# Kernel optimization log

Measured on AMD Instinct MI355X. Metric: run time of the kernel, lower is better.

The kernel has to match this reference:

```python
import jax, jax.numpy as jnp
import numpy as np

B, CI, CO = 2, 32, 32
NX, NY, NZ = 64, 64, 64
M1, M2, M3 = 8, 8, 8
ZH = NZ // 2 + 1


def _dft_mat(N, sign):
    # Dense DFT twiddle matrix W[k, n] = exp(sign * 2j*pi*k*n/N), complex64.
    a = jnp.arange(N)
    ph = (sign * 2.0) * jnp.pi * jnp.outer(a, a).astype(jnp.float32) / N
    return jnp.exp(1j * ph)


def setup_inputs() -> dict:
    key = jax.random.key(0)
    ks = jax.random.split(key, 9)
    scale = 1.0 / (CI * CO)
    x = jax.random.normal(ks[0], (B, CI, NX, NY, NZ), dtype=jnp.float32)
    wshape = (CI, CO, M1, M2, M3)
    names = ['w1r', 'w1i', 'w2r', 'w2i', 'w3r', 'w3i', 'w4r', 'w4i']
    out = {'x': x}
    for i, nm in enumerate(names):
        out[nm] = scale * jax.random.uniform(ks[i + 1], wshape, dtype=jnp.float32)
    return out


def _dht3(x):
    # Naive O(N^2)-per-axis 3D DFT via dense matmuls; return real part.
    Wx = _dft_mat(NX, -1)
    Wy = _dft_mat(NY, -1)
    Wz = _dft_mat(NZ, -1)
    y = x.astype(jnp.complex64)
    y = jnp.einsum('bcxyz,xa->bcayz', y, Wx)
    y = jnp.einsum('bcxyz,ya->bcxaz', y, Wy)
    y = jnp.einsum('bcxyz,za->bcxya', y, Wz)
    return y.real


def _idht3(X):
    # Inverse DFT via dense matmuls; rectangular (ZH -> NZ) on last axis.
    Wxi = _dft_mat(NX, +1) / NX
    Wyi = _dft_mat(NY, +1) / NY
    kz = jnp.arange(ZH)
    nz = jnp.arange(NZ)
    Wzi = jnp.exp(1j * (2.0 * jnp.pi * jnp.outer(kz, nz).astype(jnp.float32) / NZ)) / NZ
    y = jnp.einsum('bcxyz,xa->bcayz', X, Wxi)
    y = jnp.einsum('bcxyz,ya->bcxaz', y, Wyi)
    y = jnp.einsum('bcxyz,za->bcxya', y, Wzi)
    return y.real


def _mul(a, b):
    # compl_mul3d: contract over input channels in the mode block.
    return jnp.einsum('bixyz,ioxyz->boxyz', a, b)


def reference(x, w1r, w1i, w2r, w2i, w3r, w3i, w4r, w4i):
    w1 = w1r + 1j * w1i
    w2 = w2r + 1j * w2i
    w3 = w3r + 1j * w3i
    w4 = w4r + 1j * w4i

    xd = _dht3(x)  # [B, CI, NX, NY, NZ] real

    out = jnp.zeros((B, CO, NX, NY, ZH), dtype=jnp.complex64)
    out = out.at[:, :, :M1, :M2, :M3].set(_mul(xd[:, :, :M1, :M2, :M3], w1))
    out = out.at[:, :, NX - M1:, :M2, :M3].set(_mul(xd[:, :, NX - M1:, :M2, :M3], w2))
    out = out.at[:, :, :M1, NY - M2:, :M3].set(_mul(xd[:, :, :M1, NY - M2:, :M3], w3))
    out = out.at[:, :, NX - M1:, NY - M2:, :M3].set(_mul(xd[:, :, NX - M1:, NY - M2:, :M3], w4))

    return _idht3(out)  # [B, CO, NX, NY, NZ] real
```

## Files before the change

### kernel.cpp

```cpp
#include <hip/hip_runtime.h>

#define PI2_64 0.098174770424681038f


__global__ __launch_bounds__(256) void k_fwd_zy(const float* __restrict__ x,
                                                float* __restrict__ z2) {
  __shared__ __align__(16) float sp[64 * 65];
  __shared__ __align__(8) float2 Zc[64 * 9];
  __shared__ __align__(8) float2 Ec[32 * 9], Oc[32 * 9];
  __shared__ __align__(8) float2 cs[64];
  int tid = threadIdx.x;

  const float4* xg = (const float4*)(x + (long)blockIdx.x * 4096);
#pragma unroll
  for (int j = 0; j < 4; ++j) {
    int idx = j * 256 + tid;
    float4 v = xg[idx];
    int flat = idx << 2;
    int y = flat >> 6, z = flat & 63;
    float* d = &sp[y * 65 + z];
    d[0] = v.x; d[1] = v.y; d[2] = v.z; d[3] = v.w;
  }
  if (tid < 64) {
    float s, c; __sincosf(PI2_64 * (float)tid, &s, &c);
    cs[tid] = make_float2(c, s);
  }
  __syncthreads();

  {
    int y = tid >> 2, qp = tid & 3;
    const float* row = &sp[y * 65];
    float Sr[8] = {0,0,0,0,0,0,0,0}, So[8] = {0,0,0,0,0,0,0,0};
    int p0 = qp * 8 + 1, pend = (qp == 3) ? 32 : (p0 + 8);
    for (int p = p0; p < pend; ++p) {
      float a = row[p], b = row[64 - p];
      float e = a + b, o = a - b;
      Sr[0] += e;
      int m = p & 63;
#pragma unroll
      for (int k = 1; k < 8; ++k) {
        float2 t = cs[m];
        Sr[k] = fmaf(e, t.x, Sr[k]);
        So[k] = fmaf(o, t.y, So[k]);
        m = (m + p) & 63;
      }
    }
    if (qp == 3) {
      float x0 = row[0], x32 = row[32];
      float a = x0 + x32, b = x0 - x32;
#pragma unroll
      for (int k = 0; k < 8; ++k) Sr[k] += (k & 1) ? b : a;
    }
#pragma unroll
    for (int k = 0; k < 8; ++k) {
      Sr[k] += __shfl_xor(Sr[k], 1); So[k] += __shfl_xor(So[k], 1);
      Sr[k] += __shfl_xor(Sr[k], 2); So[k] += __shfl_xor(So[k], 2);
    }
    if (qp == 0) {
#pragma unroll
      for (int k = 0; k < 8; ++k) Zc[y * 9 + k] = make_float2(Sr[k], -So[k]);
    }
  }
  __syncthreads();

  if (tid < 248) {
    int yp = (tid >> 3) + 1, k = tid & 7;
    float2 a = Zc[yp * 9 + k], b = Zc[(64 - yp) * 9 + k];
    Ec[yp * 9 + k] = make_float2(a.x + b.x, a.y + b.y);
    Oc[yp * 9 + k] = make_float2(a.x - b.x, a.y - b.y);
  }
  __syncthreads();

  {
    int jp = tid >> 5, kz = (tid >> 2) & 7, h = tid & 3;
    int j = jp + 1;
    float S1 = 0, S2 = 0, S3 = 0, S4 = 0, S0r = 0, S0i = 0;
    int p0 = h * 8 + 1, pend = (h == 3) ? 32 : (p0 + 8);
    int m = (j * p0) & 63;
    for (int yp = p0; yp < pend; ++yp) {
      float2 E = Ec[yp * 9 + kz], O = Oc[yp * 9 + kz];
      float2 t = cs[m];
      S1 = fmaf(E.x, t.x, S1);
      S2 = fmaf(O.y, t.y, S2);
      S3 = fmaf(E.y, t.x, S3);
      S4 = fmaf(O.x, t.y, S4);
      if (jp == 7) { S0r += E.x; S0i += E.y; }
      m = (m + j) & 63;
    }
    if (h == 3) {
      float2 z0 = Zc[kz], z32 = Zc[32 * 9 + kz];
      float sg = (j & 1) ? -1.f : 1.f;
      S1 += z0.x + sg * z32.x;
      S3 += z0.y + sg * z32.y;
      if (jp == 7) { S0r += z0.x + z32.x; S0i += z0.y + z32.y; }
    }
    S1 += __shfl_xor(S1, 1); S1 += __shfl_xor(S1, 2);
    S2 += __shfl_xor(S2, 1); S2 += __shfl_xor(S2, 2);
    S3 += __shfl_xor(S3, 1); S3 += __shfl_xor(S3, 2);
    S4 += __shfl_xor(S4, 1); S4 += __shfl_xor(S4, 2);
    S0r += __shfl_xor(S0r, 1); S0r += __shfl_xor(S0r, 2);
    S0i += __shfl_xor(S0i, 1); S0i += __shfl_xor(S0i, 2);
    if (h == 0) {
      float2* gz = (float2*)z2 + (long)blockIdx.x * 128;
      float2 vA = (jp < 7) ? make_float2(S1 + S2, S3 - S4) : make_float2(S0r, S0i);
      int tA = (jp < 7) ? j : 0;
      float2 vB = make_float2(S1 - S2, S3 + S4);
      gz[tA * 8 + kz] = vA;
      gz[(16 - j) * 8 + kz] = vB;
    }
  }
}

__global__ __launch_bounds__(128) void k_fwd_x(const float* __restrict__ z2,
                                               float* __restrict__ xc) {
  __shared__ __align__(16) float s[64 * 16];
  int tid = threadIdx.x;
  int bi = blockIdx.x >> 4;
  int u = blockIdx.x & 15;
  const float* src = z2 + (long)bi * 16384 + u * 16;
  {
    int xr = tid >> 1, c0 = (tid & 1) * 8;
    const float4* p = (const float4*)(src + xr * 256 + c0);
    float4* q = (float4*)(s + xr * 16 + c0);
    q[0] = p[0]; q[1] = p[1];
  }
  __syncthreads();
  int t = tid >> 3, v = tid & 7;
  int f = (t < 8) ? t : 48 + t;
  float bs, bc; __sincosf(-PI2_64 * (float)f, &bs, &bc);
  float wr = 1.f, wi = 0.f, acc = 0.f;
  for (int xx = 0; xx < 64; ++xx) {
    float zr = s[xx * 16 + v * 2], zi = s[xx * 16 + v * 2 + 1];
    acc += zr * wr - zi * wi;
    float nr = wr * bc - wi * bs;
    wi = wr * bs + wi * bc;
    wr = nr;
  }
  xc[(long)bi * 2048 + t * 128 + u * 8 + v] = acc;
}

__global__ __launch_bounds__(256) void k_mix(const float* __restrict__ xc,
    const float* __restrict__ w1r, const float* __restrict__ w1i,
    const float* __restrict__ w2r, const float* __restrict__ w2i,
    const float* __restrict__ w3r, const float* __restrict__ w3i,
    const float* __restrict__ w4r, const float* __restrict__ w4i,
    float* __restrict__ outm) {
  __shared__ float sx[2 * 256];
  int tid = threadIdx.x;
  int b = blockIdx.x >> 7;
  int t = (blockIdx.x >> 3) & 15;
  int uh = blockIdx.x & 7;
  int u0 = uh * 2;
  {
    int i = tid >> 3, v = tid & 7;
    long base = (long)(b * 32 + i) * 2048 + t * 128;
    sx[tid]       = xc[base + u0 * 8 + v];
    sx[256 + tid] = xc[base + (u0 + 1) * 8 + v];
  }
  __syncthreads();
  const float* wr_ = (t < 8) ? ((u0 < 8) ? w1r : w3r) : ((u0 < 8) ? w2r : w4r);
  const float* wi_ = (t < 8) ? ((u0 < 8) ? w1i : w3i) : ((u0 < 8) ? w2i : w4i);
  int tm = t & 7, um0 = u0 & 7;
  int o = tid >> 3, v = tid & 7;
  long woff = (long)o * 512 + tm * 64 + um0 * 8 + v;
  float ar0 = 0, ai0 = 0, ar1 = 0, ai1 = 0;
#pragma unroll 4
  for (int i = 0; i < 32; ++i) {
    float x0 = sx[i * 8 + v], x1 = sx[256 + i * 8 + v];
    long wo = woff + (long)i * 16384;
    ar0 = fmaf(x0, wr_[wo], ar0);
    ai0 = fmaf(x0, wi_[wo], ai0);
    ar1 = fmaf(x1, wr_[wo + 8], ar1);
    ai1 = fmaf(x1, wi_[wo + 8], ai1);
  }
  long oi = (long)(b * 32 + o) * 2048 + t * 128 + u0 * 8 + v;
  ((float2*)outm)[oi] = make_float2(ar0, ai0);
  ((float2*)outm)[oi + 8] = make_float2(ar1, ai1);
}

__global__ __launch_bounds__(256) void k_inv_xyz(const float* __restrict__ outm,
                                                 float* __restrict__ out) {
  __shared__ __align__(8) float2 E1[9 * 128], O1[9 * 128];
  __shared__ __align__(16) float2 Y1c[128];
  __shared__ __align__(16) float2 Y2c[64 * 10];
  __shared__ __align__(8) float2 cs[64];
  __shared__ float rc[64], rs[64];
  __shared__ __align__(16) float2 ct3[512];
  int tid = threadIdx.x;
  int bo = blockIdx.x >> 6, xx = blockIdx.x & 63;

  if (tid < 64) {
    float s, c; __sincosf(PI2_64 * (float)tid, &s, &c);
    cs[tid] = make_float2(c, s); rc[tid] = c; rs[tid] = s;
  }
#pragma unroll
  for (int it = 0; it < 2; ++it) {
    int idx = tid + it * 256;
    int zq = idx >> 7, rem = idx & 127, v = rem >> 4, i = rem & 15;
    int m = (v * (zq * 16 + i)) & 63;
    float s, c; __sincosf(PI2_64 * (float)m, &s, &c);
    ct3[idx] = make_float2(c, s);
  }
  const float2* pg = (const float2*)outm + (long)bo * 2048;
  for (int it = 0; it < 5; ++it) {
    int idx = tid + it * 256;
    if (idx < 1152) {
      int j = idx >> 7, uv = idx & 127;
      float2 pA = pg[j * 128 + uv];
      float2 E, O;
      if (j == 0)      { E = pA; O = make_float2(0.f, 0.f); }
      else if (j == 8) { E = pA; O = make_float2(-pA.x, -pA.y); }
      else {
        float2 pB = pg[(16 - j) * 128 + uv];
        E = make_float2(pA.x + pB.x, pA.y + pB.y);
        O = make_float2(pA.x - pB.x, pA.y - pB.y);
      }
      E1[idx] = E; O1[idx] = O;
    }
  }
  __syncthreads();

  {
    int u = tid >> 4, v = (tid >> 1) & 7, h = tid & 1;
    int uv = u * 8 + v;
    float Yr = 0, Yi = 0;
    int j0 = h ? 5 : 0, j1 = h ? 9 : 5;
    for (int j = j0; j < j1; ++j) {
      float2 E = E1[(j << 7) + uv], O = O1[(j << 7) + uv];
      float2 t = cs[(j * xx) & 63];
      Yr += E.x * t.x - O.y * t.y;
      Yi += E.y * t.x + O.x * t.y;
    }
    Yr += __shfl_xor(Yr, 1); Yi += __shfl_xor(Yi, 1);
    if (h == 0) Y1c[uv] = make_float2(Yr, Yi);
  }
  __syncthreads();

  {
    int y = tid & 63, vq = tid >> 6, v0 = vq * 2;
    float4 A0 = *(const float4*)(&Y1c[v0]);
    float Yr0 = A0.x, Yi0 = A0.y, Yr1 = A0.z, Yi1 = A0.w;
#pragma unroll
    for (int j = 1; j < 8; ++j) {
      float4 Aj = *(const float4*)(&Y1c[j * 8 + v0]);
      float4 Bj = *(const float4*)(&Y1c[(16 - j) * 8 + v0]);
      int m = (j * y) & 63;
      float c = rc[m], s = rs[m];
      float E0r = Aj.x + Bj.x, E0i = Aj.y + Bj.y;
      float O0r = Aj.x - Bj.x, O0i = Aj.y - Bj.y;
      float E1r = Aj.z + Bj.z, E1i = Aj.w + Bj.w;
      float O1r = Aj.z - Bj.z, O1i = Aj.w - Bj.w;
      Yr0 += E0r * c - O0i * s; Yi0 += E0i * c + O0r * s;
      Yr1 += E1r * c - O1i * s; Yi1 += E1i * c + O1r * s;
    }
    {
      float4 Aj = *(const float4*)(&Y1c[64 + v0]);
      int m = (y * 8) & 63;
      float c = rc[m], s = rs[m];
      Yr0 += Aj.x * c + Aj.y * s; Yi0 += Aj.y * c - Aj.x * s;
      Yr1 += Aj.z * c + Aj.w * s; Yi1 += Aj.w * c - Aj.z * s;
    }
    const float sc = 1.f / 262144.f;
    *(float4*)(&Y2c[y * 10 + v0]) =
        make_float4(Yr0 * sc, Yi0 * sc, Yr1 * sc, Yi1 * sc);
  }
  __syncthreads();

  {
    int y = tid & 63, zq = tid >> 6;
    const float4* rowp = (const float4*)(&Y2c[y * 10]);
    float4 r0 = rowp[0], r1 = rowp[1], r2 = rowp[2], r3 = rowp[3];
    float Yr[8] = {r0.x, r0.z, r1.x, r1.z, r2.x, r2.z, r3.x, r3.z};
    float Yi[8] = {r0.y, r0.w, r1.y, r1.w, r2.y, r2.w, r3.y, r3.w};
    float acc[16];
#pragma unroll
    for (int i = 0; i < 16; ++i) acc[i] = 0.f;
#pragma unroll
    for (int v = 0; v < 8; ++v) {
      const float2* ct = &ct3[(zq * 8 + v) * 16];
#pragma unroll
      for (int i = 0; i < 16; ++i) {
        float2 t = ct[i];
        acc[i] = fmaf(Yr[v], t.x, fmaf(-Yi[v], t.y, acc[i]));
      }
    }
    float* ob = out + (long)blockIdx.x * 4096 + y * 64 + zq * 16;
#pragma unroll
    for (int q = 0; q < 4; ++q)
      ((float4*)ob)[q] = make_float4(acc[q*4], acc[q*4+1], acc[q*4+2], acc[q*4+3]);
  }
}

extern "C" void kernel_launch(void* const* d_in, const int* in_sizes, int n_in,
                              void* d_out, int out_size, void* d_ws, size_t ws_size,
                              hipStream_t stream) {
  (void)in_sizes; (void)n_in; (void)out_size; (void)ws_size;
  const float* x   = (const float*)d_in[0];
  const float* w1r = (const float*)d_in[1];
  const float* w1i = (const float*)d_in[2];
  const float* w2r = (const float*)d_in[3];
  const float* w2i = (const float*)d_in[4];
  const float* w3r = (const float*)d_in[5];
  const float* w3i = (const float*)d_in[6];
  const float* w4r = (const float*)d_in[7];
  const float* w4i = (const float*)d_in[8];
  float* out = (float*)d_out;
  float* ws = (float*)d_ws;

  float* z2   = ws;
  float* xc   = ws + 1048576;
  float* outm = ws + 1179648;

  k_fwd_zy <<<dim3(4096), dim3(256), 0, stream>>>(x, z2);
  k_fwd_x  <<<dim3(1024), dim3(128), 0, stream>>>(z2, xc);
  k_mix    <<<dim3(256),  dim3(256), 0, stream>>>(xc, w1r, w1i, w2r, w2i,
                                                  w3r, w3i, w4r, w4i, outm);
  k_inv_xyz<<<dim3(4096), dim3(256), 0, stream>>>(outm, out);
}
```

Baseline: 184.4 us.

## Replace shared-memory twiddle tables with register recurrences across FFT stages

The forward z-pass now has each thread take a contiguous 16-element chunk and build its twiddles with a per-thread rotation recurrence, instead of the even/odd symmetric split that read a cos/sin table from shared memory. The separate even/odd pass and its barrier are gone, and the y-pass now forms E/O on the fly. The x-pass is rewritten to exploit real-output symmetry, producing two outputs per thread pair, and the inverse z-pass replaces the precomputed ct3 table with a register rotation recurrence. The aim is to cut shared-memory traffic, barriers and table setup, at the cost of extra FLOPs and possible accumulated rounding error from the recurrences.

```diff
diff --git a/kernel.cpp b/kernel.cpp
--- a/kernel.cpp
+++ b/kernel.cpp
@@ -5,69 +5,59 @@
 
 __global__ __launch_bounds__(256) void k_fwd_zy(const float* __restrict__ x,
                                                 float* __restrict__ z2) {
-  __shared__ __align__(16) float sp[64 * 65];
-  __shared__ __align__(8) float2 Zc[64 * 9];
-  __shared__ __align__(8) float2 Ec[32 * 9], Oc[32 * 9];
-  __shared__ __align__(8) float2 cs[64];
+  __shared__ __align__(16) float sp[64 * 68];
+  __shared__ __align__(8) float2 Zs[64 * 9];
   int tid = threadIdx.x;
 
   const float4* xg = (const float4*)(x + (long)blockIdx.x * 4096);
 #pragma unroll
-  for (int j = 0; j < 4; ++j) {
-    int idx = j * 256 + tid;
-    float4 v = xg[idx];
-    int flat = idx << 2;
-    int y = flat >> 6, z = flat & 63;
-    float* d = &sp[y * 65 + z];
+  for (int r = 0; r < 4; ++r) {
+    int q = tid + 256 * r;
+    float4 v = xg[q];
+    int fl = q << 2;
+    int y = fl >> 6, z = fl & 63;
+    float* d = &sp[y * 68 + z];
     d[0] = v.x; d[1] = v.y; d[2] = v.z; d[3] = v.w;
   }
-  if (tid < 64) {
-    float s, c; __sincosf(PI2_64 * (float)tid, &s, &c);
-    cs[tid] = make_float2(c, s);
-  }
-  __syncthreads();
-
-  {
-    int y = tid >> 2, qp = tid & 3;
-    const float* row = &sp[y * 65];
-    float Sr[8] = {0,0,0,0,0,0,0,0}, So[8] = {0,0,0,0,0,0,0,0};
-    int p0 = qp * 8 + 1, pend = (qp == 3) ? 32 : (p0 + 8);
-    for (int p = p0; p < pend; ++p) {
-      float a = row[p], b = row[64 - p];
-      float e = a + b, o = a - b;
-      Sr[0] += e;
-      int m = p & 63;
-#pragma unroll
-      for (int k = 1; k < 8; ++k) {
-        float2 t = cs[m];
-        Sr[k] = fmaf(e, t.x, Sr[k]);
-        So[k] = fmaf(o, t.y, So[k]);
-        m = (m + p) & 63;
+  __syncthreads();
+
+  {
+    int y = tid >> 2, zq = tid & 3;
+    const float4* row = (const float4*)(&sp[y * 68 + zq * 16]);
+    float4 a0 = row[0], a1 = row[1], a2 = row[2], a3 = row[3];
+    float xr[16] = {a0.x,a0.y,a0.z,a0.w, a1.x,a1.y,a1.z,a1.w,
+                    a2.x,a2.y,a2.z,a2.w, a3.x,a3.y,a3.z,a3.w};
+    float cr[8], ci[8], sc[8], ss[8];
+#pragma unroll
+    for (int k = 0; k < 8; ++k) {
+      int m = (k * zq) & 3;
+      cr[k] = (m == 0) ? 1.f : ((m == 2) ? -1.f : 0.f);
+      ci[k] = (m == 1) ? -1.f : ((m == 3) ? 1.f : 0.f);
+      float s, c; __sincosf(PI2_64 * (float)k, &s, &c);
+      sc[k] = c; ss[k] = s;
+    }
+    float Zr[8] = {0,0,0,0,0,0,0,0}, Zi[8] = {0,0,0,0,0,0,0,0};
+#pragma unroll
+    for (int i = 0; i < 16; ++i) {
+      float xv = xr[i];
+#pragma unroll
+      for (int k = 0; k < 8; ++k) {
+        Zr[k] = fmaf(xv, cr[k], Zr[k]);
+        Zi[k] = fmaf(xv, ci[k], Zi[k]);
+        float nr = cr[k] * sc[k] + ci[k] * ss[k];
+        ci[k] = ci[k] * sc[k] - cr[k] * ss[k];
+        cr[k] = nr;
       }
     }
-    if (qp == 3) {
-      float x0 = row[0], x32 = row[32];
-      float a = x0 + x32, b = x0 - x32;
-#pragma unroll
-      for (int k = 0; k < 8; ++k) Sr[k] += (k & 1) ? b : a;
-    }
 #pragma unroll
     for (int k = 0; k < 8; ++k) {
-      Sr[k] += __shfl_xor(Sr[k], 1); So[k] += __shfl_xor(So[k], 1);
-      Sr[k] += __shfl_xor(Sr[k], 2); So[k] += __shfl_xor(So[k], 2);
-    }
-    if (qp == 0) {
-#pragma unroll
-      for (int k = 0; k < 8; ++k) Zc[y * 9 + k] = make_float2(Sr[k], -So[k]);
-    }
-  }
-  __syncthreads();
-
-  if (tid < 248) {
-    int yp = (tid >> 3) + 1, k = tid & 7;
-    float2 a = Zc[yp * 9 + k], b = Zc[(64 - yp) * 9 + k];
-    Ec[yp * 9 + k] = make_float2(a.x + b.x, a.y + b.y);
-    Oc[yp * 9 + k] = make_float2(a.x - b.x, a.y - b.y);
+      Zr[k] += __shfl_xor(Zr[k], 1); Zr[k] += __shfl_xor(Zr[k], 2);
+      Zi[k] += __shfl_xor(Zi[k], 1); Zi[k] += __shfl_xor(Zi[k], 2);
+    }
+    if (zq == 0) {
+#pragma unroll
+      for (int k = 0; k < 8; ++k) Zs[y * 9 + k] = make_float2(Zr[k], Zi[k]);
+    }
   }
   __syncthreads();
 
@@ -75,23 +65,23 @@
     int jp = tid >> 5, kz = (tid >> 2) & 7, h = tid & 3;
     int j = jp + 1;
     float S1 = 0, S2 = 0, S3 = 0, S4 = 0, S0r = 0, S0i = 0;
-    int p0 = h * 8 + 1, pend = (h == 3) ? 32 : (p0 + 8);
-    int m = (j * p0) & 63;
-    for (int yp = p0; yp < pend; ++yp) {
-      float2 E = Ec[yp * 9 + kz], O = Oc[yp * 9 + kz];
-      float2 t = cs[m];
-      S1 = fmaf(E.x, t.x, S1);
-      S2 = fmaf(O.y, t.y, S2);
-      S3 = fmaf(E.y, t.x, S3);
-      S4 = fmaf(O.x, t.y, S4);
-      if (jp == 7) { S0r += E.x; S0i += E.y; }
-      m = (m + j) & 63;
+    int p0 = 8 * h + 1, pend = (h == 3) ? 32 : (p0 + 8);
+    float c, s, stc, sts;
+    __sincosf(PI2_64 * (float)((j * p0) & 63), &s, &c);
+    __sincosf(PI2_64 * (float)j, &sts, &stc);
+    for (int p = p0; p < pend; ++p) {
+      float2 za = Zs[p * 9 + kz], zb = Zs[(64 - p) * 9 + kz];
+      float Ex = za.x + zb.x, Ey = za.y + zb.y;
+      float Ox = za.x - zb.x, Oy = za.y - zb.y;
+      S1 = fmaf(Ex, c, S1); S2 = fmaf(Oy, s, S2);
+      S3 = fmaf(Ey, c, S3); S4 = fmaf(Ox, s, S4);
+      if (jp == 7) { S0r += Ex; S0i += Ey; }
+      float nc = c * stc - s * sts; s = c * sts + s * stc; c = nc;
     }
     if (h == 3) {
-      float2 z0 = Zc[kz], z32 = Zc[32 * 9 + kz];
+      float2 z0 = Zs[kz], z32 = Zs[32 * 9 + kz];
       float sg = (j & 1) ? -1.f : 1.f;
-      S1 += z0.x + sg * z32.x;
-      S3 += z0.y + sg * z32.y;
+      S1 += z0.x + sg * z32.x; S3 += z0.y + sg * z32.y;
       if (jp == 7) { S0r += z0.x + z32.x; S0i += z0.y + z32.y; }
     }
     S1 += __shfl_xor(S1, 1); S1 += __shfl_xor(S1, 2);
@@ -104,39 +94,55 @@
       float2* gz = (float2*)z2 + (long)blockIdx.x * 128;
       float2 vA = (jp < 7) ? make_float2(S1 + S2, S3 - S4) : make_float2(S0r, S0i);
       int tA = (jp < 7) ? j : 0;
-      float2 vB = make_float2(S1 - S2, S3 + S4);
       gz[tA * 8 + kz] = vA;
-      gz[(16 - j) * 8 + kz] = vB;
+      gz[(16 - j) * 8 + kz] = make_float2(S1 - S2, S3 + S4);
     }
   }
 }
 
 __global__ __launch_bounds__(128) void k_fwd_x(const float* __restrict__ z2,
                                                float* __restrict__ xc) {
-  __shared__ __align__(16) float s[64 * 16];
+  __shared__ __align__(16) float2 Zs[64 * 10];
   int tid = threadIdx.x;
   int bi = blockIdx.x >> 4;
   int u = blockIdx.x & 15;
-  const float* src = z2 + (long)bi * 16384 + u * 16;
-  {
-    int xr = tid >> 1, c0 = (tid & 1) * 8;
-    const float4* p = (const float4*)(src + xr * 256 + c0);
-    float4* q = (float4*)(s + xr * 16 + c0);
-    q[0] = p[0]; q[1] = p[1];
-  }
-  __syncthreads();
-  int t = tid >> 3, v = tid & 7;
-  int f = (t < 8) ? t : 48 + t;
-  float bs, bc; __sincosf(-PI2_64 * (float)f, &bs, &bc);
-  float wr = 1.f, wi = 0.f, acc = 0.f;
-  for (int xx = 0; xx < 64; ++xx) {
-    float zr = s[xx * 16 + v * 2], zi = s[xx * 16 + v * 2 + 1];
-    acc += zr * wr - zi * wi;
-    float nr = wr * bc - wi * bs;
-    wi = wr * bs + wi * bc;
-    wr = nr;
-  }
-  xc[(long)bi * 2048 + t * 128 + u * 8 + v] = acc;
+  const float4* src = (const float4*)(z2 + (long)bi * 16384 + u * 16);
+#pragma unroll
+  for (int r = 0; r < 2; ++r) {
+    int q = tid + 128 * r;
+    int xx = q >> 2, pt = q & 3;
+    float4 v = src[xx * 64 + pt];
+    *(float4*)((float*)Zs + xx * 20 + pt * 4) = v;
+  }
+  __syncthreads();
+  int jp = tid >> 4, v = (tid >> 1) & 7, h = tid & 1;
+  int j = jp + 1;
+  float S1 = 0, S2 = 0, S0 = 0;
+  int p0 = 16 * h + 1, pend = (h == 1) ? 32 : 17;
+  float c, s, stc, sts;
+  __sincosf(PI2_64 * (float)((j * p0) & 63), &s, &c);
+  __sincosf(PI2_64 * (float)j, &sts, &stc);
+  for (int p = p0; p < pend; ++p) {
+    float2 za = Zs[p * 10 + v], zb = Zs[(64 - p) * 10 + v];
+    float Ex = za.x + zb.x, Oy = za.y - zb.y;
+    S1 = fmaf(Ex, c, S1); S2 = fmaf(Oy, s, S2);
+    if (jp == 7) S0 += Ex;
+    float nc = c * stc - s * sts; s = c * sts + s * stc; c = nc;
+  }
+  if (h == 1) {
+    float2 z0 = Zs[v], z32 = Zs[32 * 10 + v];
+    float sg = (j & 1) ? -1.f : 1.f;
+    S1 += z0.x + sg * z32.x;
+    if (jp == 7) S0 += z0.x + z32.x;
+  }
+  S1 += __shfl_xor(S1, 1);
+  S2 += __shfl_xor(S2, 1);
+  S0 += __shfl_xor(S0, 1);
+  if (h == 0) {
+    float* xb = xc + (long)bi * 2048 + u * 8 + v;
+    if (jp < 7) xb[j * 128] = S1 + S2; else xb[0] = S0;
+    xb[(16 - j) * 128] = S1 - S2;
+  }
 }
 
 __global__ __launch_bounds__(256) void k_mix(const float* __restrict__ xc,
@@ -185,21 +191,12 @@
   __shared__ __align__(16) float2 Y2c[64 * 10];
   __shared__ __align__(8) float2 cs[64];
   __shared__ float rc[64], rs[64];
-  __shared__ __align__(16) float2 ct3[512];
   int tid = threadIdx.x;
   int bo = blockIdx.x >> 6, xx = blockIdx.x & 63;
 
   if (tid < 64) {
     float s, c; __sincosf(PI2_64 * (float)tid, &s, &c);
     cs[tid] = make_float2(c, s); rc[tid] = c; rs[tid] = s;
-  }
-#pragma unroll
-  for (int it = 0; it < 2; ++it) {
-    int idx = tid + it * 256;
-    int zq = idx >> 7, rem = idx & 127, v = rem >> 4, i = rem & 15;
-    int m = (v * (zq * 16 + i)) & 63;
-    float s, c; __sincosf(PI2_64 * (float)m, &s, &c);
-    ct3[idx] = make_float2(c, s);
   }
   const float2* pg = (const float2*)outm + (long)bo * 2048;
   for (int it = 0; it < 5; ++it) {
@@ -277,11 +274,15 @@
     for (int i = 0; i < 16; ++i) acc[i] = 0.f;
 #pragma unroll
     for (int v = 0; v < 8; ++v) {
-      const float2* ct = &ct3[(zq * 8 + v) * 16];
+      int m = (v * zq) & 3;
+      float c = (m == 0) ? 1.f : ((m == 2) ? -1.f : 0.f);
+      float s = (m == 1) ? 1.f : ((m == 3) ? -1.f : 0.f);
+      float stc, sts; __sincosf(PI2_64 * (float)v, &sts, &stc);
+      float yr = Yr[v], yi = Yi[v];
 #pragma unroll
       for (int i = 0; i < 16; ++i) {
-        float2 t = ct[i];
-        acc[i] = fmaf(Yr[v], t.x, fmaf(-Yi[v], t.y, acc[i]));
+        acc[i] = fmaf(yr, c, fmaf(-yi, s, acc[i]));
+        float nc = c * stc - s * sts; s = c * sts + s * stc; c = nc;
       }
     }
     float* ob = out + (long)blockIdx.x * 4096 + y * 64 + zq * 16;
```

Result: no change. 183.6 us (-0.5%).
